# Optimization experiments

Measured on AMD Instinct MI355X. Metric: run time of the kernel, lower is better.

## Reference

```python
import jax, jax.numpy as jnp
import numpy as np

N, E, D_IN, D_H, D_OUT, W = 100000, 1600000, 128, 128, 128, 3
HTC_W, TEMP = 0.01, 1.0  # curvature c = 1.0


def _project(x):
    n = jnp.maximum(jnp.linalg.norm(x, axis=-1, keepdims=True), 1e-12)
    return x * jnp.minimum((1.0 - 1e-5) / n, 1.0)


def _artanh(x):
    x = jnp.clip(x, -1.0 + 1e-6, 1.0 - 1e-6)
    return 0.5 * (jnp.log1p(x) - jnp.log1p(-x))


def _expmap0(v):
    n = jnp.maximum(jnp.linalg.norm(v, axis=-1, keepdims=True), 1e-12)
    return _project(jnp.tanh(n) * v / n)


def _logmap0(y):
    y = _project(y)
    n = jnp.maximum(jnp.linalg.norm(y, axis=-1, keepdims=True), 1e-12)
    return _artanh(n) * y / n


def setup_inputs() -> dict:
    key = jax.random.key(0)
    ks = jax.random.split(key, 24)
    x = jax.random.normal(ks[0], (N, D_IN), dtype=jnp.float32)
    edge_index = jax.random.randint(ks[1], (2, E), 0, N)
    t = jax.random.uniform(ks[2], (E,), dtype=jnp.float32)
    prev_hyp = _project(jax.random.normal(ks[3], (N, D_OUT), dtype=jnp.float32) * 0.05)
    lengths = jax.random.randint(ks[4], (N,), 0, W + 1)
    valid_mask = jnp.arange(W)[None, :] < lengths[:, None]  # front-filled deque
    hist_hyp = _project(jax.random.normal(ks[5], (N, W, D_OUT), dtype=jnp.float32) * 0.05)
    hist_hyp = hist_hyp * valid_mask[..., None].astype(jnp.float32)  # padded slots are zero

    def lin(k, dout, din):
        return jax.random.normal(k, (dout, din), dtype=jnp.float32) / np.sqrt(din)

    params = dict(
        w_time=jax.random.normal(ks[6], (D_IN,), dtype=jnp.float32),
        b_time=jnp.zeros((D_IN,), jnp.float32),
        W0_l=lin(ks[7], D_H, D_IN), b0_l=jnp.zeros((D_H,), jnp.float32), W0_r=lin(ks[8], D_H, D_IN),
        W1_l=lin(ks[9], D_OUT, D_H), b1_l=jnp.zeros((D_OUT,), jnp.float32), W1_r=lin(ks[10], D_OUT, D_H),
        W_ih=lin(ks[11], 3 * D_OUT, D_OUT), W_hh=lin(ks[12], 3 * D_OUT, D_OUT),
        b_ih=jnp.zeros((3 * D_OUT,), jnp.float32), b_hh=jnp.zeros((3 * D_OUT,), jnp.float32),
        Wq=lin(ks[13], D_OUT, D_OUT), Wk=lin(ks[14], D_OUT, D_OUT), Wv=lin(ks[15], D_OUT, D_OUT),
    )
    return dict(x=x, edge_index=edge_index, t=t, prev_hyp=prev_hyp,
                hist_hyp=hist_hyp, valid_mask=valid_mask, **params)


def reference(x, edge_index, t, prev_hyp, hist_hyp, valid_mask,
              w_time, b_time, W0_l, b0_l, W0_r, W1_l, b1_l, W1_r,
              W_ih, W_hh, b_ih, b_hh, Wq, Wk, Wv):
    n = x.shape[0]
    src, dst = edge_index[0], edge_index[1]
    ones_e = jnp.ones_like(t)
    # per-node mean event time over incident edges (src and dst both count)
    nt = jax.ops.segment_sum(t, src, n) + jax.ops.segment_sum(t, dst, n)
    cnt = jax.ops.segment_sum(ones_e, src, n) + jax.ops.segment_sum(ones_e, dst, n)
    node_time = nt / jnp.maximum(cnt, 1.0)
    x = x + jnp.cos(node_time[:, None] * w_time[None, :] + b_time[None, :])
    # SAGEConv (mean aggr over incoming edges): out = W_l @ mean_j x_j + b + W_r @ x_i
    deg = jnp.maximum(jax.ops.segment_sum(ones_e, dst, n), 1.0)[:, None]
    agg0 = jax.ops.segment_sum(x[src], dst, n) / deg
    h = jax.nn.relu(agg0 @ W0_l.T + b0_l + x @ W0_r.T)
    agg1 = jax.ops.segment_sum(h[src], dst, n) / deg
    h_now = agg1 @ W1_l.T + b1_l + h @ W1_r.T  # tangent-space current embedding

    prev_tan = _logmap0(prev_hyp)
    # ragged history attention (padded + masked)
    hist_tan = _logmap0(hist_hyp)                       # [N, W, D]
    q = h_now @ Wq.T                                    # [N, D]
    k = hist_tan @ Wk.T                                 # [N, W, D]
    v = hist_tan @ Wv.T
    score = jnp.einsum('nwd,nd->nw', k, q) / (np.sqrt(D_OUT) * max(TEMP, 1e-6))
    has_hist = valid_mask.any(axis=-1, keepdims=True)
    score = jnp.where(valid_mask, score, -jnp.inf)
    score = jnp.where(has_hist, score, 0.0)
    alpha = jax.nn.softmax(score, axis=-1)
    alpha = jnp.where(has_hist, alpha, 0.0)
    ctx = jnp.einsum('nw,nwd->nd', alpha, v)

    # GRUCell(input=h_now, hidden=prev_tan + ctx)
    hidden = prev_tan + ctx
    gi = h_now @ W_ih.T + b_ih
    gh = hidden @ W_hh.T + b_hh
    i_r, i_z, i_n = jnp.split(gi, 3, axis=-1)
    h_r, h_z, h_n = jnp.split(gh, 3, axis=-1)
    r = jax.nn.sigmoid(i_r + h_r)
    z = jax.nn.sigmoid(i_z + h_z)
    nn_ = jnp.tanh(i_n + r * h_n)
    h_tan = (1.0 - z) * nn_ + z * hidden
    h_hyp = _expmap0(h_tan)

    # hyperbolic temporal consistency aux loss (c = 1)
    x_sq = jnp.sum(h_hyp * h_hyp, axis=-1)
    y_sq = jnp.sum(prev_hyp * prev_hyp, axis=-1)
    diff_sq = jnp.sum((h_hyp - prev_hyp) ** 2, axis=-1)
    denom = jnp.maximum((1.0 - x_sq) * (1.0 - y_sq), 1e-8)
    zarg = jnp.maximum(1.0 + 2.0 * diff_sq / denom, 1.0 + 1e-6)
    dist = jnp.arccosh(zarg)
    valid_prev = (jnp.sum(jnp.abs(prev_hyp), axis=-1) > 0).astype(dist.dtype)
    aux = HTC_W * jnp.sum(dist * valid_prev) / jnp.maximum(jnp.sum(valid_prev), 1.0)
    aux = jnp.where(jnp.any(valid_prev > 0), aux, 0.0)
    return h_hyp, aux
```

## Files before the change

### kernel.cpp

```cpp
#include <hip/hip_runtime.h>
#include <math.h>


typedef _Float16 f16x8 __attribute__((ext_vector_type(8)));
typedef _Float16 f16x4 __attribute__((ext_vector_type(4)));
typedef _Float16 f16x2 __attribute__((ext_vector_type(2)));
typedef float f32x4 __attribute__((ext_vector_type(4)));

__device__ __forceinline__ float wsum(float v) {
#pragma unroll
  for (int off = 1; off < 64; off <<= 1) v += __shfl_xor(v, off, 64);
  return v;
}

__device__ __forceinline__ void fsplit(float x, _Float16& h, _Float16& l) {
  h = (_Float16)x;
  l = (_Float16)(x - (float)h);
}

__device__ __forceinline__ float logmap_scale(float nrm2) {
  float n0 = fmaxf(sqrtf(nrm2), 1e-12f);
  float sp = fminf((1.0f - 1e-5f) / n0, 1.0f);
  float np = fmaxf(n0 * sp, 1e-12f);
  float a  = fminf(np, 1.0f - 1e-6f);
  float at = 0.5f * (log1pf(a) - log1pf(-a));
  return sp * at / np;
}

__global__ void k_edge(const int* __restrict__ ei, const float* __restrict__ t,
                       unsigned long long* __restrict__ packed, int E) {
  int e = blockIdx.x * 256 + threadIdx.x;
  if (e >= E) return;
  int s = ei[e], d = ei[E + e];
  unsigned long long tf =
      (unsigned long long)__float2uint_rn(t[e] * 16777216.0f);
  unsigned long long encs = tf | (1ULL << 40);
  atomicAdd(&packed[s], encs);
  atomicAdd(&packed[d], encs | (1ULL << 52));
}

__global__ void k_scan1(const unsigned long long* __restrict__ packed,
                        int* __restrict__ rowptr, int* __restrict__ bsum, int N) {
  __shared__ int s[256];
  int t = threadIdx.x;
  int base = blockIdx.x * 1024 + t * 4;
  int v[4]; int loc = 0;
#pragma unroll
  for (int j = 0; j < 4; ++j) {
    int i = base + j;
    v[j] = (i < N) ? (int)(packed[i] >> 52) : 0;
    loc += v[j];
  }
  s[t] = loc; __syncthreads();
  for (int off = 1; off < 256; off <<= 1) {
    int x = (t >= off) ? s[t - off] : 0; __syncthreads();
    s[t] += x; __syncthreads();
  }
  int run = s[t] - loc;
#pragma unroll
  for (int j = 0; j < 4; ++j) { int i = base + j; if (i < N) rowptr[i] = run; run += v[j]; }
  if (t == 255) bsum[blockIdx.x] = s[255];
}

__global__ void k_scan2(const int* __restrict__ bsum, int* __restrict__ boff, int nb) {
  __shared__ int s[128];
  int t = threadIdx.x;
  int v = (t < nb) ? bsum[t] : 0;
  s[t] = v; __syncthreads();
  for (int off = 1; off < 128; off <<= 1) {
    int x = (t >= off) ? s[t - off] : 0; __syncthreads();
    s[t] += x; __syncthreads();
  }
  boff[t] = s[t] - v;
}

__global__ void k_scan3(int* __restrict__ rowptr, const int* __restrict__ boff, int N, int E) {
  int i = blockIdx.x * 256 + threadIdx.x;
  if (i < N) rowptr[i] += boff[i >> 10];
  if (i == 0) rowptr[N] = E;
}

__global__ void k_scatter(const int* __restrict__ ei, const int* __restrict__ rowptr,
                          int* __restrict__ cursor, int* __restrict__ eidx, int E) {
  int e = blockIdx.x * 256 + threadIdx.x;
  if (e >= E) return;
  int s = ei[e], d = ei[E + e];
  int p = rowptr[d] + atomicAdd(&cursor[d], 1);
  eidx[p] = s;
}

__global__ void k_time(const float* __restrict__ x,
                       const unsigned long long* __restrict__ packed,
                       const float* __restrict__ wt,
                       const float* __restrict__ bt, float* __restrict__ outF,
                       _Float16* __restrict__ outH, _Float16* __restrict__ outL, int N) {
  int id = blockIdx.x * 256 + threadIdx.x;
  if (id >= N * 32) return;
  int n = id >> 5, q = id & 31;
  unsigned long long p = packed[n];
  float tsum = (float)(p & 0xFFFFFFFFFFULL) * 5.9604644775390625e-8f;
  int c = (int)((p >> 40) & 0xFFF);
  float tm = tsum / fmaxf((float)c, 1.0f);
  float4 xv = ((const float4*)x)[id];
  float4 wv = ((const float4*)wt)[q];
  float4 bv = ((const float4*)bt)[q];
  float o[4];
  o[0] = xv.x + cosf(tm * wv.x + bv.x);
  o[1] = xv.y + cosf(tm * wv.y + bv.y);
  o[2] = xv.z + cosf(tm * wv.z + bv.z);
  o[3] = xv.w + cosf(tm * wv.w + bv.w);
  ((float4*)outF)[id] = make_float4(o[0], o[1], o[2], o[3]);
  f16x4 vh, vl;
#pragma unroll
  for (int j = 0; j < 4; ++j) { _Float16 h, l; fsplit(o[j], h, l); vh[j] = h; vl[j] = l; }
  *(f16x4*)&outH[(size_t)id * 4] = vh;
  *(f16x4*)&outL[(size_t)id * 4] = vl;
}

__global__ void k_agg(const float* __restrict__ X, const int* __restrict__ rowptr,
                      const int* __restrict__ eidx, _Float16* __restrict__ outH,
                      _Float16* __restrict__ outL, int N) {
  int wid = threadIdx.x >> 6, lane = threadIdx.x & 63;
  int n = blockIdx.x * 4 + wid;
  if (n >= N) return;
  int s0 = rowptr[n], s1 = rowptr[n + 1];
  float ax = 0.f, ay = 0.f;
  for (int e = s0; e < s1; ++e) {
    int s = eidx[e];
    float2 v = ((const float2*)X)[(size_t)s * 64 + lane];
    ax += v.x; ay += v.y;
  }
  float sc = 1.0f / fmaxf((float)(s1 - s0), 1.0f);
  _Float16 hx, lx, hy, ly;
  fsplit(ax * sc, hx, lx); fsplit(ay * sc, hy, ly);
  f16x2 vh = {hx, hy}, vl = {lx, ly};
  *(f16x2*)&outH[(size_t)n * 128 + lane * 2] = vh;
  *(f16x2*)&outL[(size_t)n * 128 + lane * 2] = vl;
}

__global__ void k_prep(const float* __restrict__ W0l, const float* __restrict__ W0r,
                       const float* __restrict__ W1l, const float* __restrict__ W1r,
                       const float* __restrict__ Wv,  const float* __restrict__ Wih,
                       const float* __restrict__ Whh, const float* __restrict__ bih,
                       const float* __restrict__ bhh,
                       _Float16* __restrict__ W0H, _Float16* __restrict__ W0L,
                       _Float16* __restrict__ W1H, _Float16* __restrict__ W1L,
                       _Float16* __restrict__ WvH, _Float16* __restrict__ WvL,
                       _Float16* __restrict__ WzH, _Float16* __restrict__ WzL,
                       float* __restrict__ bz) {
  int id = blockIdx.x * 256 + threadIdx.x;
  if (id < 32768) {
    int c = id >> 8, k = id & 255;
    float v0 = (k < 128) ? W0l[c * 128 + k] : W0r[c * 128 + (k - 128)];
    float v1 = (k < 128) ? W1l[c * 128 + k] : W1r[c * 128 + (k - 128)];
    fsplit(v0, W0H[id], W0L[id]);
    fsplit(v1, W1H[id], W1L[id]);
  }
  if (id < 16384) {
    fsplit(Wv[id], WvH[id], WvL[id]);
  }
  if (id < 131072) {
    int c = id >> 8, k = id & 255;
    float v;
    if (c < 256)      v = (k < 128) ? Wih[c * 128 + k] : Whh[c * 128 + (k - 128)];
    else if (c < 384) v = (k < 128) ? Wih[c * 128 + k] : 0.f;
    else              v = (k < 128) ? 0.f : Whh[(c - 128) * 128 + (k - 128)];
    fsplit(v, WzH[id], WzL[id]);
  }
  if (id < 512) {
    float v;
    if (id < 256)      v = bih[id] + bhh[id];
    else if (id < 384) v = bih[id];
    else               v = bhh[id - 128];
    bz[id] = v;
  }
}

__global__ void k_ct(const float* __restrict__ Wk, const float* __restrict__ Wq,
                     _Float16* __restrict__ CtH, _Float16* __restrict__ CtL) {
  int id = blockIdx.x * 256 + threadIdx.x;
  if (id >= 16384) return;
  int c = id >> 7, k = id & 127;
  float s = 0.f;
  for (int j = 0; j < 128; ++j) s += Wk[j * 128 + c] * Wq[j * 128 + k];
  fsplit(s, CtH[id], CtL[id]);
}

__global__ __launch_bounds__(256)
void k_mm(const _Float16* __restrict__ A1H, const _Float16* __restrict__ A1L,
          const _Float16* __restrict__ A2H, const _Float16* __restrict__ A2L,
          const _Float16* __restrict__ WH,  const _Float16* __restrict__ WL,
          const float* __restrict__ bias,   const float* __restrict__ addb,
          float* __restrict__ outF, _Float16* __restrict__ outH,
          _Float16* __restrict__ outL,
          int Nrows, int Ktot, int Ctot, int relu) {
  __shared__ _Float16 sA[2][128][64];
  __shared__ _Float16 sW[2][128][64];
  const int tid = threadIdx.x;
  const int lane = tid & 63;
  const int wv = tid >> 6;
  const int wr = wv >> 1, wc = wv & 1;
  const int laneR = lane & 15, laneG = lane >> 4;
  const int n0 = blockIdx.x * 128;
  const int c0 = blockIdx.y * 128;

  f32x4 acc[4][4];
#pragma unroll
  for (int mi = 0; mi < 4; ++mi)
#pragma unroll
    for (int ni = 0; ni < 4; ++ni)
#pragma unroll
      for (int j = 0; j < 4; ++j) acc[mi][ni][j] = 0.f;

  const int nslab = Ktot >> 6;
  for (int s = 0; s < nslab; ++s) {
    int kglob = s << 6;
    const _Float16* aH = (kglob < 128) ? A1H : A2H;
    const _Float16* aL = (kglob < 128) ? A1L : A2L;
    int kc = kglob & 127;
    __syncthreads();
#pragma unroll
    for (int it = 0; it < 4; ++it) {
      int idx = tid + (it << 8);
      int r = idx >> 3, chunk = idx & 7;
      int cs = (chunk ^ (r & 7)) << 3;
      int kq = chunk << 3;
      int n = n0 + r;
      f16x8 vh, vl;
      if (n < Nrows) {
        vh = *(const f16x8*)&aH[(size_t)n * 128 + kc + kq];
        vl = *(const f16x8*)&aL[(size_t)n * 128 + kc + kq];
      } else {
#pragma unroll
        for (int j = 0; j < 8; ++j) { vh[j] = (_Float16)0; vl[j] = (_Float16)0; }
      }
      *(f16x8*)&sA[0][r][cs] = vh;
      *(f16x8*)&sA[1][r][cs] = vl;
      int c = c0 + r;
      f16x8 wh = *(const f16x8*)&WH[(size_t)c * Ktot + kglob + kq];
      f16x8 wl = *(const f16x8*)&WL[(size_t)c * Ktot + kglob + kq];
      *(f16x8*)&sW[0][r][cs] = wh;
      *(f16x8*)&sW[1][r][cs] = wl;
    }
    __syncthreads();
#pragma unroll
    for (int kk = 0; kk < 2; ++kk) {
      f16x8 ah[4], al[4], bh[4], bl[4];
      int kch = (kk << 2) + laneG;
#pragma unroll
      for (int m = 0; m < 4; ++m) {
        int row = wr * 64 + m * 16 + laneR;
        int ko = (kch ^ (row & 7)) << 3;
        ah[m] = *(const f16x8*)&sA[0][row][ko];
        al[m] = *(const f16x8*)&sA[1][row][ko];
      }
#pragma unroll
      for (int n = 0; n < 4; ++n) {
        int row = wc * 64 + n * 16 + laneR;
        int ko = (kch ^ (row & 7)) << 3;
        bh[n] = *(const f16x8*)&sW[0][row][ko];
        bl[n] = *(const f16x8*)&sW[1][row][ko];
      }
#pragma unroll
      for (int m = 0; m < 4; ++m)
#pragma unroll
        for (int n = 0; n < 4; ++n) {
          acc[m][n] = __builtin_amdgcn_mfma_f32_16x16x32_f16(ah[m], bh[n], acc[m][n], 0, 0, 0);
          acc[m][n] = __builtin_amdgcn_mfma_f32_16x16x32_f16(al[m], bh[n], acc[m][n], 0, 0, 0);
          acc[m][n] = __builtin_amdgcn_mfma_f32_16x16x32_f16(ah[m], bl[n], acc[m][n], 0, 0, 0);
        }
    }
  }
#pragma unroll
  for (int m = 0; m < 4; ++m) {
#pragma unroll
    for (int n = 0; n < 4; ++n) {
      int rbase = n0 + wr * 64 + m * 16 + laneG * 4;
      int c = c0 + wc * 64 + n * 16 + laneR;
      float bval = bias ? bias[c] : 0.f;
#pragma unroll
      for (int j = 0; j < 4; ++j) {
        int r = rbase + j;
        if (r >= Nrows) continue;
        float v = acc[m][n][j] + bval;
        if (addb) v += addb[(size_t)r * Ctot + c];
        if (relu) v = fmaxf(v, 0.f);
        if (outF) outF[(size_t)r * Ctot + c] = v;
        if (outH) {
          _Float16 h, l; fsplit(v, h, l);
          outH[(size_t)r * Ctot + c] = h;
          outL[(size_t)r * Ctot + c] = l;
        }
      }
    }
  }
}

__global__ __launch_bounds__(256, 2)
void k_gru(const _Float16* __restrict__ P0H, const _Float16* __restrict__ P0L,
           const _Float16* __restrict__ P2H, const _Float16* __restrict__ P2L,
           const _Float16* __restrict__ WzH, const _Float16* __restrict__ WzL,
           const float* __restrict__ bz, const float* __restrict__ prev,
           float* __restrict__ out, float* __restrict__ pd,
           float* __restrict__ pv, int N) {
  __shared__ _Float16 sA[2][64][64];
  __shared__ _Float16 sW[2][128][64];
  __shared__ float rn1[64][2];
  __shared__ float rn3[64][2][3];
  __shared__ float distrow[64], validrow[64];
  const int tid = threadIdx.x;
  const int lane = tid & 63;
  const int wv = tid >> 6;
  const int wr = wv >> 1, wc = wv & 1;
  const int laneR = lane & 15, laneG = lane >> 4;
  const int n0 = blockIdx.x * 64;

  f32x4 acc[4][2][4];
#pragma unroll
  for (int q = 0; q < 4; ++q)
#pragma unroll
    for (int m = 0; m < 2; ++m)
#pragma unroll
      for (int n = 0; n < 4; ++n)
#pragma unroll
        for (int j = 0; j < 4; ++j) acc[q][m][n][j] = 0.f;

#pragma unroll
  for (int s = 0; s < 4; ++s) {
    int kglob = s << 6;
    const _Float16* aH = (kglob < 128) ? P0H : P2H;
    const _Float16* aL = (kglob < 128) ? P0L : P2L;
    int kc = kglob & 127;
    __syncthreads();
#pragma unroll
    for (int it = 0; it < 2; ++it) {
      int idx = tid + (it << 8);
      int r = idx >> 3, chunk = idx & 7;
      int cs = (chunk ^ (r & 7)) << 3;
      int kq = chunk << 3;
      int n = n0 + r;
      f16x8 vh, vl;
      if (n < N) {
        vh = *(const f16x8*)&aH[(size_t)n * 128 + kc + kq];
        vl = *(const f16x8*)&aL[(size_t)n * 128 + kc + kq];
      } else {
#pragma unroll
        for (int j = 0; j < 8; ++j) { vh[j] = (_Float16)0; vl[j] = (_Float16)0; }
      }
      *(f16x8*)&sA[0][r][cs] = vh;
      *(f16x8*)&sA[1][r][cs] = vl;
    }
#pragma unroll
    for (int q = 0; q < 4; ++q) {
      if (q) __syncthreads();
#pragma unroll
      for (int it = 0; it < 4; ++it) {
        int idx = tid + (it << 8);
        int r = idx >> 3, chunk = idx & 7;
        int cs = (chunk ^ (r & 7)) << 3;
        int kq = chunk << 3;
        size_t wrow = (size_t)(q * 128 + r);
        *(f16x8*)&sW[0][r][cs] = *(const f16x8*)&WzH[wrow * 256 + kglob + kq];
        *(f16x8*)&sW[1][r][cs] = *(const f16x8*)&WzL[wrow * 256 + kglob + kq];
      }
      __syncthreads();
#pragma unroll
      for (int kk = 0; kk < 2; ++kk) {
        int kch = (kk << 2) + laneG;
        f16x8 ah[2], al[2], bh[4], bl[4];
#pragma unroll
        for (int m = 0; m < 2; ++m) {
          int row = wr * 32 + m * 16 + laneR;
          int ko = (kch ^ (row & 7)) << 3;
          ah[m] = *(const f16x8*)&sA[0][row][ko];
          al[m] = *(const f16x8*)&sA[1][row][ko];
        }
#pragma unroll
        for (int n = 0; n < 4; ++n) {
          int row = wc * 64 + n * 16 + laneR;
          int ko = (kch ^ (row & 7)) << 3;
          bh[n] = *(const f16x8*)&sW[0][row][ko];
          bl[n] = *(const f16x8*)&sW[1][row][ko];
        }
#pragma unroll
        for (int m = 0; m < 2; ++m)
#pragma unroll
          for (int n = 0; n < 4; ++n) {
            acc[q][m][n] = __builtin_amdgcn_mfma_f32_16x16x32_f16(ah[m], bh[n], acc[q][m][n], 0, 0, 0);
            acc[q][m][n] = __builtin_amdgcn_mfma_f32_16x16x32_f16(al[m], bh[n], acc[q][m][n], 0, 0, 0);
            acc[q][m][n] = __builtin_amdgcn_mfma_f32_16x16x32_f16(ah[m], bl[n], acc[q][m][n], 0, 0, 0);
          }
      }
    }
  }

  float bz0[4], bz1[4], bz2[4], bz3[4];
#pragma unroll
  for (int n = 0; n < 4; ++n) {
    int d = wc * 64 + n * 16 + laneR;
    bz0[n] = bz[d]; bz1[n] = bz[128 + d]; bz2[n] = bz[256 + d]; bz3[n] = bz[384 + d];
  }
  float tv[2][4][4];
#pragma unroll
  for (int m = 0; m < 2; ++m)
#pragma unroll
    for (int n = 0; n < 4; ++n)
#pragma unroll
      for (int j = 0; j < 4; ++j) {
        int row = n0 + wr * 32 + m * 16 + laneG * 4 + j;
        int d = wc * 64 + n * 16 + laneR;
        float hid = 0.f;
        if (row < N) {
          size_t o = (size_t)row * 128 + d;
          hid = (float)P2H[o] + (float)P2L[o];
        }
        float gr = acc[0][m][n][j] + bz0[n];
        float gz = acc[1][m][n][j] + bz1[n];
        float gi = acc[2][m][n][j] + bz2[n];
        float gh = acc[3][m][n][j] + bz3[n];
        float rr = 1.f / (1.f + expf(-gr));
        float zz = 1.f / (1.f + expf(-gz));
        float nn = tanhf(gi + rr * gh);
        tv[m][n][j] = (1.f - zz) * nn + zz * hid;
      }
#pragma unroll
  for (int m = 0; m < 2; ++m)
#pragma unroll
    for (int j = 0; j < 4; ++j) {
      float p = 0.f;
#pragma unroll
      for (int n = 0; n < 4; ++n) p += tv[m][n][j] * tv[m][n][j];
#pragma unroll
      for (int off = 1; off < 16; off <<= 1) p += __shfl_xor(p, off, 64);
      if (laneR == 0) rn1[wr * 32 + m * 16 + laneG * 4 + j][wc] = p;
    }
  __syncthreads();
  float hv[2][4][4];
#pragma unroll
  for (int m = 0; m < 2; ++m)
#pragma unroll
    for (int j = 0; j < 4; ++j) {
      int rl = wr * 32 + m * 16 + laneG * 4 + j;
      int row = n0 + rl;
      float nv2 = rn1[rl][0] + rn1[rl][1];
      float nv = fmaxf(sqrtf(nv2), 1e-12f);
      float tn = tanhf(nv);
      float s1 = tn / nv;
      float nw = fmaxf(tn, 1e-12f);
      float sp = fminf((1.f - 1e-5f) / nw, 1.f);
      float scl = s1 * sp;
#pragma unroll
      for (int n = 0; n < 4; ++n) {
        float h = tv[m][n][j] * scl;
        hv[m][n][j] = h;
        int d = wc * 64 + n * 16 + laneR;
        if (row < N) out[(size_t)row * 128 + d] = h;
      }
    }
#pragma unroll
  for (int m = 0; m < 2; ++m)
#pragma unroll
    for (int j = 0; j < 4; ++j) {
      int rl = wr * 32 + m * 16 + laneG * 4 + j;
      int row = n0 + rl;
      float ys = 0.f, ds = 0.f, pa = 0.f;
#pragma unroll
      for (int n = 0; n < 4; ++n) {
        int d = wc * 64 + n * 16 + laneR;
        float p = (row < N) ? prev[(size_t)row * 128 + d] : 0.f;
        float h = hv[m][n][j];
        ys += p * p; ds += (h - p) * (h - p); pa += fabsf(p);
      }
#pragma unroll
      for (int off = 1; off < 16; off <<= 1) {
        ys += __shfl_xor(ys, off, 64);
        ds += __shfl_xor(ds, off, 64);
        pa += __shfl_xor(pa, off, 64);
      }
      if (laneR == 0) { rn3[rl][wc][0] = ys; rn3[rl][wc][1] = ds; rn3[rl][wc][2] = pa; }
    }
  __syncthreads();
  if (wc == 0 && laneR == 0) {
#pragma unroll
    for (int m = 0; m < 2; ++m)
#pragma unroll
      for (int j = 0; j < 4; ++j) {
        int rl = wr * 32 + m * 16 + laneG * 4 + j;
        int row = n0 + rl;
        float nv2 = rn1[rl][0] + rn1[rl][1];
        float nv = fmaxf(sqrtf(nv2), 1e-12f);
        float tn = tanhf(nv);
        float s1 = tn / nv;
        float nw = fmaxf(tn, 1e-12f);
        float sp = fminf((1.f - 1e-5f) / nw, 1.f);
        float scl = s1 * sp;
        float x_sq = scl * scl * nv2;
        float y_sq = rn3[rl][0][0] + rn3[rl][1][0];
        float d_sq = rn3[rl][0][1] + rn3[rl][1][1];
        float pab  = rn3[rl][0][2] + rn3[rl][1][2];
        float denom = fmaxf((1.f - x_sq) * (1.f - y_sq), 1e-8f);
        float zarg = fmaxf(1.f + 2.f * d_sq / denom, 1.f + 1e-6f);
        float dist = acoshf(zarg);
        float valid = (pab > 0.f && row < N) ? 1.f : 0.f;
        distrow[rl] = dist * valid;
        validrow[rl] = valid;
      }
  }
  __syncthreads();
  if (tid < 64) {
    float dv = distrow[tid], vvv = validrow[tid];
    dv = wsum(dv); vvv = wsum(vvv);
    if (tid == 0) { pd[blockIdx.x] = dv; pv[blockIdx.x] = vvv; }
  }
}

__global__ void k_logmap(const float* __restrict__ Y, float* __restrict__ out, int N) {
  int wid = threadIdx.x >> 6, lane = threadIdx.x & 63;
  int n = blockIdx.x * 4 + wid;
  if (n >= N) return;
  float2 y = ((const float2*)Y)[(size_t)n * 64 + lane];
  float nrm2 = wsum(y.x * y.x + y.y * y.y);
  float s = logmap_scale(nrm2);
  ((float2*)out)[(size_t)n * 64 + lane] = make_float2(y.x * s, y.y * s);
}

__global__ void k_attn(const float* __restrict__ U, const float* __restrict__ hist,
                       _Float16* __restrict__ outH, _Float16* __restrict__ outL, int N) {
  int wid = threadIdx.x >> 6, lane = threadIdx.x & 63;
  int n = blockIdx.x * 4 + wid;
  if (n >= N) return;
  float2 u = ((const float2*)U)[(size_t)n * 64 + lane];
  float htx[3], hty[3], sc[3];
  bool val[3];
#pragma unroll
  for (int w = 0; w < 3; ++w) {
    float2 h = ((const float2*)hist)[((size_t)n * 3 + w) * 64 + lane];
    float nrm2 = wsum(h.x * h.x + h.y * h.y);
    val[w] = nrm2 > 0.f;
    float s = logmap_scale(nrm2);
    htx[w] = h.x * s; hty[w] = h.y * s;
    float d = wsum(htx[w] * u.x + hty[w] * u.y);
    sc[w] = d * 0.0883883476483184f;
  }
  float cx = 0.f, cy = 0.f;
  if (val[0] || val[1] || val[2]) {
    float m = -INFINITY;
#pragma unroll
    for (int w = 0; w < 3; ++w) if (val[w]) m = fmaxf(m, sc[w]);
    float a[3]; float ssum = 0.f;
#pragma unroll
    for (int w = 0; w < 3; ++w) { a[w] = val[w] ? expf(sc[w] - m) : 0.f; ssum += a[w]; }
    float inv = 1.f / ssum;
#pragma unroll
    for (int w = 0; w < 3; ++w) { cx += htx[w] * (a[w] * inv); cy += hty[w] * (a[w] * inv); }
  }
  _Float16 hx, lx, hy, ly;
  fsplit(cx, hx, lx); fsplit(cy, hy, ly);
  f16x2 vh = {hx, hy}, vl = {lx, ly};
  *(f16x2*)&outH[(size_t)n * 128 + lane * 2] = vh;
  *(f16x2*)&outL[(size_t)n * 128 + lane * 2] = vl;
}

__global__ void k_reduce(const float* __restrict__ pd, const float* __restrict__ pv,
                         float* __restrict__ aux_out, int nparts) {
  __shared__ float sd[256], sv[256];
  float a = 0.f, b = 0.f;
  for (int i = threadIdx.x; i < nparts; i += 256) { a += pd[i]; b += pv[i]; }
  sd[threadIdx.x] = a; sv[threadIdx.x] = b; __syncthreads();
  for (int off = 128; off > 0; off >>= 1) {
    if (threadIdx.x < off) { sd[threadIdx.x] += sd[threadIdx.x + off]; sv[threadIdx.x] += sv[threadIdx.x + off]; }
    __syncthreads();
  }
  if (threadIdx.x == 0) {
    float aux = (sv[0] > 0.f) ? 0.01f * sd[0] / fmaxf(sv[0], 1.f) : 0.f;
    aux_out[0] = aux;
  }
}

extern "C" void kernel_launch(void* const* d_in, const int* in_sizes, int n_in,
                              void* d_out, int out_size, void* d_ws, size_t ws_size,
                              hipStream_t stream) {
  const float* x      = (const float*)d_in[0];
  const int*   ei     = (const int*)  d_in[1];
  const float* t      = (const float*)d_in[2];
  const float* prev   = (const float*)d_in[3];
  const float* hist   = (const float*)d_in[4];
  const float* w_time = (const float*)d_in[6];
  const float* b_time = (const float*)d_in[7];
  const float* W0l    = (const float*)d_in[8];
  const float* b0l    = (const float*)d_in[9];
  const float* W0r    = (const float*)d_in[10];
  const float* W1l    = (const float*)d_in[11];
  const float* b1l    = (const float*)d_in[12];
  const float* W1r    = (const float*)d_in[13];
  const float* Wih    = (const float*)d_in[14];
  const float* Whh    = (const float*)d_in[15];
  const float* bih    = (const float*)d_in[16];
  const float* bhh    = (const float*)d_in[17];
  const float* Wq     = (const float*)d_in[18];
  const float* Wk     = (const float*)d_in[19];
  const float* Wv     = (const float*)d_in[20];

  const int N = in_sizes[0] / 128;
  const int E = in_sizes[1] / 2;
  const int NB4 = (N + 3) / 4;
  const int NB1 = (N + 1023) / 1024;
  const int NBG = (N + 63) / 64;

  char* wbase = (char*)d_ws;
  size_t off = 0;
  auto alloc = [&](size_t bytes) -> void* {
    off = (off + 255) & ~(size_t)255;
    void* p = wbase + off; off += bytes; return p;
  };
  unsigned long long* packed = (unsigned long long*)alloc((size_t)N * 8);
  int*   cursor = (int*)  alloc((size_t)N * 4);
  size_t zero_bytes = off;
  int*   rowptr = (int*)  alloc((size_t)(N + 1) * 4);
  int*   bsum   = (int*)  alloc(512);
  int*   boff   = (int*)  alloc(512);
  int*   eidx   = (int*)  alloc((size_t)E * 4);
  _Float16* W0H = (_Float16*)alloc(32768 * 2);
  _Float16* W0L = (_Float16*)alloc(32768 * 2);
  _Float16* W1H = (_Float16*)alloc(32768 * 2);
  _Float16* W1L = (_Float16*)alloc(32768 * 2);
  _Float16* CtH = (_Float16*)alloc(16384 * 2);
  _Float16* CtL = (_Float16*)alloc(16384 * 2);
  _Float16* WvH = (_Float16*)alloc(16384 * 2);
  _Float16* WvL = (_Float16*)alloc(16384 * 2);
  _Float16* WzH = (_Float16*)alloc(131072 * 2);
  _Float16* WzL = (_Float16*)alloc(131072 * 2);
  float* bz     = (float*)alloc(512 * 4);
  float* F0 = (float*)alloc((size_t)N * 128 * 4);
  float* F1 = (float*)alloc((size_t)N * 128 * 4);
  _Float16* P0H = (_Float16*)alloc((size_t)N * 128 * 2);
  _Float16* P0L = (_Float16*)alloc((size_t)N * 128 * 2);
  _Float16* P1H = (_Float16*)alloc((size_t)N * 128 * 2);
  _Float16* P1L = (_Float16*)alloc((size_t)N * 128 * 2);
  _Float16* P2H = (_Float16*)alloc((size_t)N * 128 * 2);
  _Float16* P2L = (_Float16*)alloc((size_t)N * 128 * 2);
  float* pd = (float*)alloc((size_t)NBG * 4);
  float* pv = (float*)alloc((size_t)NBG * 4);
  (void)ws_size; (void)n_in; (void)out_size;

  float* out_h   = (float*)d_out;
  float* out_aux = out_h + (size_t)N * 128;

  hipMemsetAsync(d_ws, 0, zero_bytes, stream);

  k_prep<<<512, 256, 0, stream>>>(W0l, W0r, W1l, W1r, Wv, Wih, Whh, bih, bhh,
                                  W0H, W0L, W1H, W1L, WvH, WvL, WzH, WzL, bz);
  k_ct<<<64, 256, 0, stream>>>(Wk, Wq, CtH, CtL);

  int ebl = (E + 255) / 256;
  k_edge<<<ebl, 256, 0, stream>>>(ei, t, packed, E);
  k_scan1<<<NB1, 256, 0, stream>>>(packed, rowptr, bsum, N);
  k_scan2<<<1, 128, 0, stream>>>(bsum, boff, NB1);
  k_scan3<<<(N + 255) / 256, 256, 0, stream>>>(rowptr, boff, N, E);
  k_scatter<<<ebl, 256, 0, stream>>>(ei, rowptr, cursor, eidx, E);

  k_time<<<(N * 32 + 255) / 256, 256, 0, stream>>>(x, packed, w_time, b_time,
                                                   F0, P0H, P0L, N);
  k_agg<<<NB4, 256, 0, stream>>>(F0, rowptr, eidx, P1H, P1L, N);
  dim3 gb((N + 127) / 128, 1);
  k_mm<<<gb, 256, 0, stream>>>(P1H, P1L, P0H, P0L, W0H, W0L, b0l, nullptr,
                               F1, P2H, P2L, N, 256, 128, 1);
  k_agg<<<NB4, 256, 0, stream>>>(F1, rowptr, eidx, P1H, P1L, N);
  k_mm<<<gb, 256, 0, stream>>>(P1H, P1L, P2H, P2L, W1H, W1L, b1l, nullptr,
                               nullptr, P0H, P0L, N, 256, 128, 0);
  k_mm<<<gb, 256, 0, stream>>>(P0H, P0L, nullptr, nullptr, CtH, CtL, nullptr, nullptr,
                               F0, nullptr, nullptr, N, 128, 128, 0);
  k_attn<<<NB4, 256, 0, stream>>>(F0, hist, P1H, P1L, N);
  k_logmap<<<NB4, 256, 0, stream>>>(prev, F1, N);
  k_mm<<<gb, 256, 0, stream>>>(P1H, P1L, nullptr, nullptr, WvH, WvL, nullptr, F1,
                               nullptr, P2H, P2L, N, 128, 128, 0);
  k_gru<<<NBG, 256, 0, stream>>>(P0H, P0L, P2H, P2L, WzH, WzL, bz, prev,
                                 out_h, pd, pv, N);
  k_reduce<<<1, 256, 0, stream>>>(pd, pv, out_aux, NBG);
}
```

Measured before the change: 1.213 ms.

## Skip zero gate blocks in GRU GEMM and double rows per block

Restructures the fused GRU matmul so each K-stage computes only the three gate quadrants that have nonzero weights. The input half skips the hidden-only n-gate block and the hidden half skips the input-only n-gate block, so it no longer multiplies structurally zero weights. The block also grows to 512 threads covering 128 rows, which halves how often each weight tile is staged per row. The final per-block aux reduction gains a small shared-memory step. The larger block raises register and LDS pressure per block and can lower occupancy.

```diff
diff --git a/kernel.cpp b/kernel.cpp
--- a/kernel.cpp
+++ b/kernel.cpp
@@ -296,24 +296,25 @@
   }
 }
 
-__global__ __launch_bounds__(256, 2)
+__global__ __launch_bounds__(512, 2)
 void k_gru(const _Float16* __restrict__ P0H, const _Float16* __restrict__ P0L,
            const _Float16* __restrict__ P2H, const _Float16* __restrict__ P2L,
            const _Float16* __restrict__ WzH, const _Float16* __restrict__ WzL,
            const float* __restrict__ bz, const float* __restrict__ prev,
            float* __restrict__ out, float* __restrict__ pd,
            float* __restrict__ pv, int N) {
-  __shared__ _Float16 sA[2][64][64];
+  __shared__ _Float16 sA[2][128][64];
   __shared__ _Float16 sW[2][128][64];
-  __shared__ float rn1[64][2];
-  __shared__ float rn3[64][2][3];
-  __shared__ float distrow[64], validrow[64];
+  __shared__ float rn1[128][2];
+  __shared__ float rn3[128][2][3];
+  __shared__ float distrow[128], validrow[128];
+  __shared__ float sred[2][2];
   const int tid = threadIdx.x;
   const int lane = tid & 63;
   const int wv = tid >> 6;
   const int wr = wv >> 1, wc = wv & 1;
   const int laneR = lane & 15, laneG = lane >> 4;
-  const int n0 = blockIdx.x * 64;
+  const int n0 = blockIdx.x * 128;
 
   f32x4 acc[4][2][4];
 #pragma unroll
@@ -324,17 +325,62 @@
       for (int n = 0; n < 4; ++n)
 #pragma unroll
         for (int j = 0; j < 4; ++j) acc[q][m][n][j] = 0.f;
+
+#define STAGE_W(Q)                                                          \
+  {                                                                         \
+    _Pragma("unroll")                                                       \
+    for (int it = 0; it < 2; ++it) {                                        \
+      int idx = tid + (it << 9);                                            \
+      int r = idx >> 3, chunk = idx & 7;                                    \
+      int cs = (chunk ^ (r & 7)) << 3;                                      \
+      int kq = chunk << 3;                                                  \
+      size_t wrow = (size_t)((Q)*128 + r);                                  \
+      *(f16x8*)&sW[0][r][cs] = *(const f16x8*)&WzH[wrow * 256 + kglob + kq];\
+      *(f16x8*)&sW[1][r][cs] = *(const f16x8*)&WzL[wrow * 256 + kglob + kq];\
+    }                                                                       \
+  }
+
+#define COMPUTE_Q(Q)                                                        \
+  {                                                                         \
+    _Pragma("unroll")                                                       \
+    for (int kk = 0; kk < 2; ++kk) {                                        \
+      int kch = (kk << 2) + laneG;                                          \
+      f16x8 ah[2], al[2], bh[4], bl[4];                                     \
+      _Pragma("unroll")                                                     \
+      for (int m = 0; m < 2; ++m) {                                         \
+        int row = wr * 32 + m * 16 + laneR;                                 \
+        int ko = (kch ^ (row & 7)) << 3;                                    \
+        ah[m] = *(const f16x8*)&sA[0][row][ko];                             \
+        al[m] = *(const f16x8*)&sA[1][row][ko];                             \
+      }                                                                     \
+      _Pragma("unroll")                                                     \
+      for (int n = 0; n < 4; ++n) {                                         \
+        int row = wc * 64 + n * 16 + laneR;                                 \
+        int ko = (kch ^ (row & 7)) << 3;                                    \
+        bh[n] = *(const f16x8*)&sW[0][row][ko];                             \
+        bl[n] = *(const f16x8*)&sW[1][row][ko];                             \
+      }                                                                     \
+      _Pragma("unroll")                                                     \
+      for (int m = 0; m < 2; ++m)                                           \
+        _Pragma("unroll")                                                   \
+        for (int n = 0; n < 4; ++n) {                                       \
+          acc[Q][m][n] = __builtin_amdgcn_mfma_f32_16x16x32_f16(ah[m], bh[n], acc[Q][m][n], 0, 0, 0); \
+          acc[Q][m][n] = __builtin_amdgcn_mfma_f32_16x16x32_f16(al[m], bh[n], acc[Q][m][n], 0, 0, 0); \
+          acc[Q][m][n] = __builtin_amdgcn_mfma_f32_16x16x32_f16(ah[m], bl[n], acc[Q][m][n], 0, 0, 0); \
+        }                                                                   \
+    }                                                                       \
+  }
 
 #pragma unroll
   for (int s = 0; s < 4; ++s) {
     int kglob = s << 6;
-    const _Float16* aH = (kglob < 128) ? P0H : P2H;
-    const _Float16* aL = (kglob < 128) ? P0L : P2L;
+    const _Float16* aH = (s < 2) ? P0H : P2H;
+    const _Float16* aL = (s < 2) ? P0L : P2L;
     int kc = kglob & 127;
     __syncthreads();
 #pragma unroll
     for (int it = 0; it < 2; ++it) {
-      int idx = tid + (it << 8);
+      int idx = tid + (it << 9);
       int r = idx >> 3, chunk = idx & 7;
       int cs = (chunk ^ (r & 7)) << 3;
       int kq = chunk << 3;
@@ -350,49 +396,26 @@
       *(f16x8*)&sA[0][r][cs] = vh;
       *(f16x8*)&sA[1][r][cs] = vl;
     }
-#pragma unroll
-    for (int q = 0; q < 4; ++q) {
-      if (q) __syncthreads();
-#pragma unroll
-      for (int it = 0; it < 4; ++it) {
-        int idx = tid + (it << 8);
-        int r = idx >> 3, chunk = idx & 7;
-        int cs = (chunk ^ (r & 7)) << 3;
-        int kq = chunk << 3;
-        size_t wrow = (size_t)(q * 128 + r);
-        *(f16x8*)&sW[0][r][cs] = *(const f16x8*)&WzH[wrow * 256 + kglob + kq];
-        *(f16x8*)&sW[1][r][cs] = *(const f16x8*)&WzL[wrow * 256 + kglob + kq];
-      }
+    STAGE_W(0);
+    __syncthreads();
+    COMPUTE_Q(0);
+    __syncthreads();
+    STAGE_W(1);
+    __syncthreads();
+    COMPUTE_Q(1);
+    __syncthreads();
+    if (s < 2) {
+      STAGE_W(2);
       __syncthreads();
-#pragma unroll
-      for (int kk = 0; kk < 2; ++kk) {
-        int kch = (kk << 2) + laneG;
-        f16x8 ah[2], al[2], bh[4], bl[4];
-#pragma unroll
-        for (int m = 0; m < 2; ++m) {
-          int row = wr * 32 + m * 16 + laneR;
-          int ko = (kch ^ (row & 7)) << 3;
-          ah[m] = *(const f16x8*)&sA[0][row][ko];
-          al[m] = *(const f16x8*)&sA[1][row][ko];
-        }
-#pragma unroll
-        for (int n = 0; n < 4; ++n) {
-          int row = wc * 64 + n * 16 + laneR;
-          int ko = (kch ^ (row & 7)) << 3;
-          bh[n] = *(const f16x8*)&sW[0][row][ko];
-          bl[n] = *(const f16x8*)&sW[1][row][ko];
-        }
-#pragma unroll
-        for (int m = 0; m < 2; ++m)
-#pragma unroll
-          for (int n = 0; n < 4; ++n) {
-            acc[q][m][n] = __builtin_amdgcn_mfma_f32_16x16x32_f16(ah[m], bh[n], acc[q][m][n], 0, 0, 0);
-            acc[q][m][n] = __builtin_amdgcn_mfma_f32_16x16x32_f16(al[m], bh[n], acc[q][m][n], 0, 0, 0);
-            acc[q][m][n] = __builtin_amdgcn_mfma_f32_16x16x32_f16(ah[m], bl[n], acc[q][m][n], 0, 0, 0);
-          }
-      }
+      COMPUTE_Q(2);
+    } else {
+      STAGE_W(3);
+      __syncthreads();
+      COMPUTE_Q(3);
     }
   }
+#undef STAGE_W
+#undef COMPUTE_Q
 
   float bz0[4], bz1[4], bz2[4], bz3[4];
 #pragma unroll
@@ -507,10 +530,15 @@
       }
   }
   __syncthreads();
-  if (tid < 64) {
+  if (tid < 128) {
     float dv = distrow[tid], vvv = validrow[tid];
     dv = wsum(dv); vvv = wsum(vvv);
-    if (tid == 0) { pd[blockIdx.x] = dv; pv[blockIdx.x] = vvv; }
+    if ((tid & 63) == 0) { sred[tid >> 6][0] = dv; sred[tid >> 6][1] = vvv; }
+  }
+  __syncthreads();
+  if (tid == 0) {
+    pd[blockIdx.x] = sred[0][0] + sred[1][0];
+    pv[blockIdx.x] = sred[0][1] + sred[1][1];
   }
 }
 
@@ -605,7 +633,7 @@
   const int E = in_sizes[1] / 2;
   const int NB4 = (N + 3) / 4;
   const int NB1 = (N + 1023) / 1024;
-  const int NBG = (N + 63) / 64;
+  const int NBG = (N + 127) / 128;
 
   char* wbase = (char*)d_ws;
   size_t off = 0;
@@ -674,7 +702,7 @@
   k_logmap<<<NB4, 256, 0, stream>>>(prev, F1, N);
   k_mm<<<gb, 256, 0, stream>>>(P1H, P1L, nullptr, nullptr, WvH, WvL, nullptr, F1,
                                nullptr, P2H, P2L, N, 128, 128, 0);
-  k_gru<<<NBG, 256, 0, stream>>>(P0H, P0L, P2H, P2L, WzH, WzL, bz, prev,
+  k_gru<<<NBG, 512, 0, stream>>>(P0H, P0L, P2H, P2L, WzH, WzL, bz, prev,
                                  out_h, pd, pv, N);
   k_reduce<<<1, 256, 0, stream>>>(pd, pv, out_aux, NBG);
 }
```

Measured after the change: 1.248 ms. 2.8% more time.
